# Kernel optimization log

Hardware: AMD Instinct MI355X
Metric: run time of the kernel (lower is better)

The kernel has to match this reference:

```python
import jax, jax.numpy as jnp
import numpy as np


def setup_inputs() -> dict:
    key = jax.random.key(0)
    ks = jax.random.split(key, 5)
    B, Lq, Lkv, E, H = 4, 4096, 4096, 1024, 128
    x = jax.random.normal(ks[0], (B, Lq, E), dtype=jnp.float32)
    z = jax.random.normal(ks[1], (B, Lkv, E), dtype=jnp.float32)
    s = 1.0 / np.sqrt(E)
    Wq = jax.random.normal(ks[2], (H, E), dtype=jnp.float32) * s
    Wk = jax.random.normal(ks[3], (H, E), dtype=jnp.float32) * s
    Wv = jax.random.normal(ks[4], (H, E), dtype=jnp.float32) * s
    return {"x": x, "z": z, "Wq": Wq, "Wk": Wk, "Wv": Wv}


def reference(x, z, Wq, Wk, Wv):
    # q: [B, Lq, H]; k, v: [B, Lkv, H]  (torch Linear: y = x @ W.T)
    q = jnp.einsum('bqe,he->bqh', x, Wq)
    k = jnp.einsum('bke,he->bkh', z, Wk)
    v = jnp.einsum('bke,he->bkh', z, Wv)
    # NOTE: original code MULTIPLIES by sqrt(head_dim) (faithful reproduction)
    scale = jnp.asarray(k.shape[-1], x.dtype) ** 0.5
    weights = jnp.einsum('bqh,bkh->bqk', q, k) * scale  # [B, Lq, Lkv]
    weights = jax.nn.softmax(weights, axis=-1)
    logits = jnp.einsum('bqk,bkh->bqh', weights, v)  # [B, Lq, H]
    return logits
```

## Files before the change

kernel.cpp:

```cpp
#include <hip/hip_runtime.h>

typedef __attribute__((ext_vector_type(8))) short short8;
typedef __attribute__((ext_vector_type(4))) float f32x4;
typedef __attribute__((ext_vector_type(4))) float float4v;
typedef __attribute__((ext_vector_type(4))) unsigned short ushort4v;
typedef unsigned int __attribute__((may_alias)) u32ma;

#define B_   4
#define LQ   4096
#define LKV  4096
#define E_   1024
#define H_   128
#define NSPLIT 4
#define KVSPL (LKV / NSPLIT)
#define NT    (KVSPL / 64)
#define WELEM (H_ * E_)

static __device__ __forceinline__ unsigned short bf16_rne(float f) {
    unsigned int u = __float_as_uint(f);
    u += 0x7fffu + ((u >> 16) & 1u);
    return (unsigned short)(u >> 16);
}
static __device__ __forceinline__ float bf16_tof(unsigned short h) {
    return __uint_as_float(((unsigned int)h) << 16);
}
static __device__ __forceinline__ f32x4 mfma16(short8 a, short8 b, f32x4 c) {
    return __builtin_amdgcn_mfma_f32_16x16x32_bf16(a, b, c, 0, 0, 0);
}
static __device__ __forceinline__ void gload16(const unsigned short* g, unsigned short* l) {
    __builtin_amdgcn_global_load_lds(
        (const __attribute__((address_space(1))) unsigned int*)g,
        (__attribute__((address_space(3))) unsigned int*)l, 16, 0, 0);
}

__global__ __launch_bounds__(256) void convert_w_kernel(
    const float* __restrict__ Wq, const float* __restrict__ Wk, const float* __restrict__ Wv,
    unsigned short* __restrict__ wqh, unsigned short* __restrict__ wql,
    unsigned short* __restrict__ wkh, unsigned short* __restrict__ wkl,
    unsigned short* __restrict__ wvh)
{
    const int kb = blockIdx.x;
    const int which = blockIdx.y;
    const float* W = (which == 0) ? Wq : (which == 1) ? Wk : Wv;
    unsigned short* outh = (which == 0) ? wqh : (which == 1) ? wkh : wvh;
    unsigned short* outl = (which == 0) ? wql : wkl;
    const int t = threadIdx.x;
#pragma unroll
    for (int i = 0; i < 4; ++i) {
        const int c = t * 4 + i;
        const int h = c >> 3;
        const int k = kb * 64 + (((c & 7) ^ (h & 7)) * 8);
        const float* src = W + (size_t)h * E_ + k;
        float4v v0 = *(const float4v*)(src);
        float4v v1 = *(const float4v*)(src + 4);
        short8 hi, lo;
#pragma unroll
        for (int e = 0; e < 4; ++e) {
            unsigned short h0 = bf16_rne(v0[e]);
            unsigned short h1 = bf16_rne(v1[e]);
            hi[e] = (short)h0; hi[e + 4] = (short)h1;
            lo[e] = (short)bf16_rne(v0[e] - bf16_tof(h0));
            lo[e + 4] = (short)bf16_rne(v1[e] - bf16_tof(h1));
        }
        *(short8*)&outh[(size_t)kb * 8192 + (size_t)c * 8] = hi;
        if (which < 2) *(short8*)&outl[(size_t)kb * 8192 + (size_t)c * 8] = lo;
    }
}

__global__ __launch_bounds__(512, 1) void proj_kernel(
    const float* __restrict__ x, const float* __restrict__ z,
    const unsigned short* __restrict__ wqh, const unsigned short* __restrict__ wql,
    const unsigned short* __restrict__ wkh, const unsigned short* __restrict__ wkl,
    const unsigned short* __restrict__ wvh,
    unsigned short* __restrict__ qhi, unsigned short* __restrict__ qlo,
    unsigned short* __restrict__ khi, unsigned short* __restrict__ klo,
    unsigned short* __restrict__ vt)
{
    const int bid = blockIdx.x;
    const bool qmode = bid < 128;
    const int m0 = (qmode ? bid : bid - 128) * 128;
    const float* Asrc = qmode ? x : z;
    const unsigned short* W1h = qmode ? wqh : wkh;
    const unsigned short* W1l = qmode ? wql : wkl;

    const int t = threadIdx.x;
    const int w = t >> 6, l = t & 63, lg = (l >> 4) & 3, ll = l & 15;
    const int mw = w & 3, nw = w >> 2;

    __shared__ unsigned short Ah[8192];
    __shared__ unsigned short Al[8192];
    __shared__ unsigned short Wh[2][8192];
    __shared__ unsigned short Wl[2][8192];
    __shared__ unsigned short Wv2[2][8192];

    const int ar = t >> 2, aq = t & 3;
    float4v ra[4];
    auto loadA = [&](int e0) {
        const float* p = Asrc + (size_t)(m0 + ar) * E_ + e0 + aq * 16;
#pragma unroll
        for (int i = 0; i < 4; ++i) ra[i] = *(const float4v*)(p + i * 4);
    };
    auto writeA = [&]() {
#pragma unroll
        for (int half = 0; half < 2; ++half) {
            short8 hi, lo;
#pragma unroll
            for (int e = 0; e < 4; ++e) {
                float v0 = ra[2 * half][e];
                float v1 = ra[2 * half + 1][e];
                unsigned short h0 = bf16_rne(v0);
                unsigned short h1 = bf16_rne(v1);
                hi[e] = (short)h0; hi[e + 4] = (short)h1;
                lo[e] = (short)bf16_rne(v0 - bf16_tof(h0));
                lo[e + 4] = (short)bf16_rne(v1 - bf16_tof(h1));
            }
            const int j = 2 * aq + half;
            const int off = ar * 64 + ((j ^ (ar & 7)) * 8);
            *(short8*)&Ah[off] = hi;
            *(short8*)&Al[off] = lo;
        }
    };
    auto issueW = [&](int kb, int bsel) {
#pragma unroll
        for (int i = 0; i < 2; ++i) {
            const int cbase = w * 128 + i * 64;
            const size_t so = (size_t)kb * 8192 + (size_t)(cbase + l) * 8;
            gload16(W1h + so, &Wh[bsel][(size_t)cbase * 8]);
            gload16(W1l + so, &Wl[bsel][(size_t)cbase * 8]);
            if (!qmode) gload16(wvh + so, &Wv2[bsel][(size_t)cbase * 8]);
        }
    };

    f32x4 acc[2][4], accv[2][4];
    const f32x4 zz = {0.f, 0.f, 0.f, 0.f};
#pragma unroll
    for (int rf = 0; rf < 2; ++rf)
#pragma unroll
        for (int cf = 0; cf < 4; ++cf) { acc[rf][cf] = zz; accv[rf][cf] = zz; }

    issueW(0, 0);
    loadA(0);
    writeA();
    __syncthreads();

    for (int kb = 0; kb < 16; ++kb) {
        const int bsel = kb & 1;
        if (kb < 15) { issueW(kb + 1, bsel ^ 1); loadA((kb + 1) * 64); }

#pragma unroll
        for (int ks = 0; ks < 2; ++ks) {
            short8 a_h[2], a_l[2];
#pragma unroll
            for (int rf = 0; rf < 2; ++rf) {
                const int r = mw * 32 + rf * 16 + ll;
                const int off = r * 64 + (((ks * 4 + lg) ^ (ll & 7)) * 8);
                a_h[rf] = *(const short8*)&Ah[off];
                a_l[rf] = *(const short8*)&Al[off];
            }
#pragma unroll
            for (int cf = 0; cf < 4; ++cf) {
                const int hrow = nw * 64 + cf * 16 + ll;
                const int off = hrow * 64 + (((ks * 4 + lg) ^ (ll & 7)) * 8);
                short8 bh = *(const short8*)&Wh[bsel][off];
                short8 bl = *(const short8*)&Wl[bsel][off];
#pragma unroll
                for (int rf = 0; rf < 2; ++rf) {
                    acc[rf][cf] = mfma16(a_h[rf], bh, acc[rf][cf]);
                    acc[rf][cf] = mfma16(a_h[rf], bl, acc[rf][cf]);
                    acc[rf][cf] = mfma16(a_l[rf], bh, acc[rf][cf]);
                }
                if (!qmode) {
                    short8 bv = *(const short8*)&Wv2[bsel][off];
#pragma unroll
                    for (int rf = 0; rf < 2; ++rf)
                        accv[rf][cf] = mfma16(a_h[rf], bv, accv[rf][cf]);
                }
            }
        }
        __syncthreads();
        if (kb < 15) {
            writeA();
            __syncthreads();
        }
    }

#pragma unroll
    for (int rf = 0; rf < 2; ++rf)
#pragma unroll
        for (int cf = 0; cf < 4; ++cf)
#pragma unroll
            for (int j = 0; j < 4; ++j) {
                const int m = m0 + mw * 32 + rf * 16 + 4 * lg + j;
                const int h = nw * 64 + cf * 16 + ll;
                const float val = acc[rf][cf][j];
                unsigned short hi = bf16_rne(val);
                unsigned short lo = bf16_rne(val - bf16_tof(hi));
                const size_t o = (size_t)m * H_ + h;
                if (qmode) {
                    qhi[o] = hi; qlo[o] = lo;
                } else {
                    khi[o] = hi; klo[o] = lo;
                    const int b = m >> 12, kv = m & 4095;
                    vt[(size_t)b * ((size_t)H_ * LKV) + (size_t)h * LKV + kv] =
                        bf16_rne(accv[rf][cf][j]);
                }
            }
}

__global__ __launch_bounds__(256, 2) void attn_kernel(
    const unsigned short* __restrict__ qhi, const unsigned short* __restrict__ qlo,
    const unsigned short* __restrict__ khi, const unsigned short* __restrict__ klo,
    const unsigned short* __restrict__ vt,
    float* __restrict__ Opart, float* __restrict__ msb, float* __restrict__ lsb)
{
    const int blk = blockIdx.x;
    const int bb = blk & 3;
    const int qt = (blk >> 2) & 31;
    const int split = blk >> 7;
    const int t = threadIdx.x;
    const int w = t >> 6, l = t & 63, lg = (l >> 4) & 3, ll = l & 15;

    __shared__ unsigned short Kh[8192];
    __shared__ unsigned short Kl[8192];
    __shared__ unsigned short Vb[8192];
    __shared__ unsigned short Pl[4][32][64];

    const float CSC = 11.313708498984761f * 1.4426950408889634f;

    short8 qh[2][4], ql[2][4];
#pragma unroll
    for (int b = 0; b < 2; ++b) {
        const size_t qrow = (size_t)(bb * LQ + qt * 128 + w * 32 + b * 16 + ll) * H_;
#pragma unroll
        for (int ks = 0; ks < 4; ++ks) {
            qh[b][ks] = *(const short8*)(qhi + qrow + ks * 32 + lg * 8);
            ql[b][ks] = *(const short8*)(qlo + qrow + ks * 32 + lg * 8);
        }
    }

    const int kv_base = split * KVSPL;
    const unsigned short* khb = khi + (size_t)bb * LKV * H_;
    const unsigned short* klb = klo + (size_t)bb * LKV * H_;
    const unsigned short* vbg = vt + (size_t)bb * ((size_t)H_ * LKV);

    auto issue_K = [&](int kv0) {
#pragma unroll
        for (int ci = 0; ci < 4; ++ci) {
            const int chunk = w * 4 + ci;
            const int row = chunk * 4 + (l >> 4);
            const int c = l & 15;
            const size_t so = (size_t)(kv0 + row) * H_ + ((c ^ (row & 7)) * 8);
            gload16(khb + so, &Kh[chunk * 512]);
            gload16(klb + so, &Kl[chunk * 512]);
        }
    };
    auto issue_V = [&](int kv0) {
#pragma unroll
        for (int ci = 0; ci < 4; ++ci) {
            const int chunk = w * 4 + ci;
            const int row = chunk * 8 + (l >> 3);
            const int c = l & 7;
            gload16(vbg + (size_t)row * LKV + kv0 + ((c ^ (row & 7)) * 8),
                    &Vb[chunk * 512]);
        }
    };

    f32x4 O[8][2];
    const f32x4 zz = {0.f, 0.f, 0.f, 0.f};
#pragma unroll
    for (int f = 0; f < 8; ++f) { O[f][0] = zz; O[f][1] = zz; }
    float mold[2] = {-1e30f, -1e30f};
    float lsum[2] = {0.f, 0.f};

    issue_K(kv_base);
    issue_V(kv_base);
    asm volatile("s_waitcnt vmcnt(0)" ::: "memory");
    __builtin_amdgcn_s_barrier();

    for (int ti = 0; ti < NT; ++ti) {
        f32x4 S[4][2];
#pragma unroll
        for (int a = 0; a < 4; ++a) { S[a][0] = zz; S[a][1] = zz; }
        __builtin_amdgcn_s_setprio(1);
#pragma unroll
        for (int ks = 0; ks < 4; ++ks) {
#pragma unroll
            for (int a = 0; a < 4; ++a) {
                const int row = a * 16 + ll;
                const int off = row * 128 + (((ks * 4 + lg) ^ (ll & 7)) * 8);
                short8 kh  = *(const short8*)&Kh[off];
                short8 kl2 = *(const short8*)&Kl[off];
                S[a][0] = mfma16(kh,  qh[0][ks], S[a][0]);
                S[a][0] = mfma16(kh,  ql[0][ks], S[a][0]);
                S[a][0] = mfma16(kl2, qh[0][ks], S[a][0]);
                S[a][1] = mfma16(kh,  qh[1][ks], S[a][1]);
                S[a][1] = mfma16(kh,  ql[1][ks], S[a][1]);
                S[a][1] = mfma16(kl2, qh[1][ks], S[a][1]);
            }
        }
        __builtin_amdgcn_s_setprio(0);

        float crr[2];
#pragma unroll
        for (int b = 0; b < 2; ++b) {
            float mx = S[0][b][0];
#pragma unroll
            for (int a = 0; a < 4; ++a)
#pragma unroll
                for (int j = 0; j < 4; ++j) mx = fmaxf(mx, S[a][b][j]);
            mx = fmaxf(mx, __shfl_xor(mx, 16));
            mx = fmaxf(mx, __shfl_xor(mx, 32));
            float mn = fmaxf(mold[b], mx * CSC);
            float corr = exp2f(mold[b] - mn);
            float ps = 0.f;
#pragma unroll
            for (int a = 0; a < 4; ++a) {
                float p0 = exp2f(fmaf(S[a][b][0], CSC, -mn));
                float p1 = exp2f(fmaf(S[a][b][1], CSC, -mn));
                float p2 = exp2f(fmaf(S[a][b][2], CSC, -mn));
                float p3 = exp2f(fmaf(S[a][b][3], CSC, -mn));
                ps += (p0 + p1) + (p2 + p3);
                unsigned int pk0, pk1;
                asm("v_cvt_pk_bf16_f32 %0, %1, %2" : "=v"(pk0) : "v"(p0), "v"(p1));
                asm("v_cvt_pk_bf16_f32 %0, %1, %2" : "=v"(pk1) : "v"(p2), "v"(p3));
                const int row = b * 16 + ll;
                u32ma* pd = (u32ma*)&Pl[w][0][0];
                const int di = row * 32 + (((2 * a + (lg >> 1)) ^ (ll & 7)) * 4) + 2 * (lg & 1);
                pd[di] = pk0;
                pd[di + 1] = pk1;
            }
            ps += __shfl_xor(ps, 16);
            ps += __shfl_xor(ps, 32);
            lsum[b] = lsum[b] * corr + ps;
            mold[b] = mn;
            crr[b] = corr;
        }
#pragma unroll
        for (int f = 0; f < 8; ++f) {
            O[f][0] *= crr[0];
            O[f][1] *= crr[1];
        }

        asm volatile("s_waitcnt vmcnt(0) lgkmcnt(0)" ::: "memory");
        __builtin_amdgcn_sched_barrier(0);
        __builtin_amdgcn_s_barrier();
        if (ti + 1 < NT) issue_K(kv_base + (ti + 1) * 64);
        __builtin_amdgcn_sched_barrier(0);

        __builtin_amdgcn_s_setprio(1);
#pragma unroll
        for (int ks = 0; ks < 2; ++ks) {
            short8 pb[2];
#pragma unroll
            for (int b = 0; b < 2; ++b) {
                const int row = b * 16 + ll;
                pb[b] = *(const short8*)&Pl[w][row][((ks * 4 + lg) ^ (ll & 7)) * 8];
            }
#pragma unroll
            for (int f = 0; f < 8; ++f) {
                const int row = f * 16 + ll;
                short8 va = *(const short8*)&Vb[row * 64
                                               + (((ks * 4 + lg) ^ (ll & 7)) * 8)];
                O[f][0] = mfma16(va, pb[0], O[f][0]);
                O[f][1] = mfma16(va, pb[1], O[f][1]);
            }
        }
        __builtin_amdgcn_s_setprio(0);

        __builtin_amdgcn_s_barrier();
        if (ti + 1 < NT) issue_V(kv_base + (ti + 1) * 64);
        asm volatile("s_waitcnt vmcnt(4)" ::: "memory");
        __builtin_amdgcn_sched_barrier(0);
        __builtin_amdgcn_s_barrier();
    }

    const size_t obase = ((((size_t)split * 4 + bb) * 32 + qt) * 4 + w) * 16;
#pragma unroll
    for (int f = 0; f < 8; ++f)
#pragma unroll
        for (int b = 0; b < 2; ++b)
            *(float4v*)&Opart[(obase + f * 2 + b) * 256 + l * 4] = O[f][b];

    if (lg == 0) {
#pragma unroll
        for (int b = 0; b < 2; ++b) {
            const int q = qt * 128 + w * 32 + b * 16 + ll;
            msb[((size_t)split * 4 + bb) * LQ + q] = mold[b];
            lsb[((size_t)split * 4 + bb) * LQ + q] = lsum[b];
        }
    }
}

__global__ __launch_bounds__(512) void combine_kernel(
    const float* __restrict__ Opart, const float* __restrict__ msb,
    const float* __restrict__ lsb, float* __restrict__ out)
{
    const int blk = blockIdx.x;
    const int bb = blk & 3;
    const int qt = (blk >> 2) & 31;
    const int fg = blk >> 7;
    const int t = threadIdx.x;
    const int w = t >> 6, l = t & 63, lg = (l >> 4) & 3, ll = l & 15;
    const int wq = w & 3, wf = w >> 2;

#pragma unroll
    for (int b = 0; b < 2; ++b) {
        const int q = qt * 128 + wq * 32 + b * 16 + ll;
        float ms[NSPLIT], ls[NSPLIT];
#pragma unroll
        for (int s = 0; s < NSPLIT; ++s) {
            ms[s] = msb[((size_t)s * 4 + bb) * LQ + q];
            ls[s] = lsb[((size_t)s * 4 + bb) * LQ + q];
        }
        float mM = fmaxf(fmaxf(ms[0], ms[1]), fmaxf(ms[2], ms[3]));
        float wsp[NSPLIT];
        float L = 0.f;
#pragma unroll
        for (int s = 0; s < NSPLIT; ++s) {
            wsp[s] = exp2f(ms[s] - mM);
            L += ls[s] * wsp[s];
        }
        const float inv = 1.f / L;
#pragma unroll
        for (int fi = 0; fi < 2; ++fi) {
            const int f = fg * 4 + wf * 2 + fi;
            f32x4 acc = {0.f, 0.f, 0.f, 0.f};
#pragma unroll
            for (int s = 0; s < NSPLIT; ++s) {
                const size_t ob = ((((size_t)s * 4 + bb) * 32 + qt) * 4 + wq) * 16 + f * 2 + b;
                float4v ov = *(const float4v*)&Opart[ob * 256 + l * 4];
#pragma unroll
                for (int j = 0; j < 4; ++j) acc[j] += ov[j] * wsp[s];
            }
#pragma unroll
            for (int j = 0; j < 4; ++j) acc[j] *= inv;
            *(float4v*)&out[((size_t)bb * LQ + q) * H_ + f * 16 + lg * 4] = acc;
        }
    }
}

extern "C" void kernel_launch(void* const* d_in, const int* in_sizes, int n_in,
                              void* d_out, int out_size, void* d_ws, size_t ws_size,
                              hipStream_t stream) {
    const float* x  = (const float*)d_in[0];
    const float* z  = (const float*)d_in[1];
    const float* Wq = (const float*)d_in[2];
    const float* Wk = (const float*)d_in[3];
    const float* Wv = (const float*)d_in[4];
    float* out = (float*)d_out;

    const size_t NQ = (size_t)B_ * LQ * H_;
    unsigned short* qhi = (unsigned short*)d_ws;
    unsigned short* qlo = qhi + NQ;
    unsigned short* khi = qlo + NQ;
    unsigned short* klo = khi + NQ;
    unsigned short* vtp = klo + NQ;
    float* Opart = (float*)(vtp + NQ);
    float* msb   = Opart + (size_t)NSPLIT * NQ;
    float* lsb   = msb + (size_t)NSPLIT * B_ * LQ;
    unsigned short* wqh = (unsigned short*)(lsb + (size_t)NSPLIT * B_ * LQ);
    unsigned short* wql = wqh + WELEM;
    unsigned short* wkh = wql + WELEM;
    unsigned short* wkl = wkh + WELEM;
    unsigned short* wvh = wkl + WELEM;

    convert_w_kernel<<<dim3(16, 3), 256, 0, stream>>>(Wq, Wk, Wv, wqh, wql, wkh, wkl, wvh);
    proj_kernel<<<dim3(256), 512, 0, stream>>>(x, z, wqh, wql, wkh, wkl, wvh,
                                               qhi, qlo, khi, klo, vtp);
    attn_kernel<<<dim3(512), 256, 0, stream>>>(qhi, qlo, khi, klo, vtp, Opart, msb, lsb);
    combine_kernel<<<dim3(256), 512, 0, stream>>>(Opart, msb, lsb, out);
}
```

Baseline: 138.7 us.

## Double-buffer K tiles, keep P in registers, skip unneeded softmax rescale

```diff
diff --git a/kernel.cpp b/kernel.cpp
--- a/kernel.cpp
+++ b/kernel.cpp
@@ -3,7 +3,7 @@
 typedef __attribute__((ext_vector_type(8))) short short8;
 typedef __attribute__((ext_vector_type(4))) float f32x4;
 typedef __attribute__((ext_vector_type(4))) float float4v;
-typedef __attribute__((ext_vector_type(4))) unsigned short ushort4v;
+typedef __attribute__((ext_vector_type(4))) unsigned int u32x4;
 typedef unsigned int __attribute__((may_alias)) u32ma;
 
 #define B_   4
@@ -201,7 +201,10 @@
                 } else {
                     khi[o] = hi; klo[o] = lo;
                     const int b = m >> 12, kv = m & 4095;
-                    vt[(size_t)b * ((size_t)H_ * LKV) + (size_t)h * LKV + kv] =
+                    const int kv5 = kv & 31;
+                    const int kvp = (kv & ~31) | (((kv5 >> 2) & 3) << 3)
+                                  | (((kv5 >> 4) & 1) << 2) | (kv5 & 3);
+                    vt[(size_t)b * ((size_t)H_ * LKV) + (size_t)h * LKV + kvp] =
                         bf16_rne(accv[rf][cf][j]);
                 }
             }
@@ -220,10 +223,9 @@
     const int t = threadIdx.x;
     const int w = t >> 6, l = t & 63, lg = (l >> 4) & 3, ll = l & 15;
 
-    __shared__ unsigned short Kh[8192];
-    __shared__ unsigned short Kl[8192];
+    __shared__ unsigned short Kh[2][8192];
+    __shared__ unsigned short Kl[2][8192];
     __shared__ unsigned short Vb[8192];
-    __shared__ unsigned short Pl[4][32][64];
 
     const float CSC = 11.313708498984761f * 1.4426950408889634f;
 
@@ -243,15 +245,15 @@
     const unsigned short* klb = klo + (size_t)bb * LKV * H_;
     const unsigned short* vbg = vt + (size_t)bb * ((size_t)H_ * LKV);
 
-    auto issue_K = [&](int kv0) {
+    auto issue_K = [&](int kv0, int sel) {
 #pragma unroll
         for (int ci = 0; ci < 4; ++ci) {
             const int chunk = w * 4 + ci;
             const int row = chunk * 4 + (l >> 4);
             const int c = l & 15;
             const size_t so = (size_t)(kv0 + row) * H_ + ((c ^ (row & 7)) * 8);
-            gload16(khb + so, &Kh[chunk * 512]);
-            gload16(klb + so, &Kl[chunk * 512]);
+            gload16(khb + so, &Kh[sel][chunk * 512]);
+            gload16(klb + so, &Kl[sel][chunk * 512]);
         }
     };
     auto issue_V = [&](int kv0) {
@@ -272,12 +274,16 @@
     float mold[2] = {-1e30f, -1e30f};
     float lsum[2] = {0.f, 0.f};
 
-    issue_K(kv_base);
+    issue_K(kv_base, 0);
     issue_V(kv_base);
     asm volatile("s_waitcnt vmcnt(0)" ::: "memory");
     __builtin_amdgcn_s_barrier();
 
     for (int ti = 0; ti < NT; ++ti) {
+        const int cur = ti & 1;
+        if (ti + 1 < NT) issue_K(kv_base + (ti + 1) * 64, cur ^ 1);
+        __builtin_amdgcn_sched_barrier(0);
+
         f32x4 S[4][2];
 #pragma unroll
         for (int a = 0; a < 4; ++a) { S[a][0] = zz; S[a][1] = zz; }
@@ -288,8 +294,8 @@
             for (int a = 0; a < 4; ++a) {
                 const int row = a * 16 + ll;
                 const int off = row * 128 + (((ks * 4 + lg) ^ (ll & 7)) * 8);
-                short8 kh  = *(const short8*)&Kh[off];
-                short8 kl2 = *(const short8*)&Kl[off];
+                short8 kh  = *(const short8*)&Kh[cur][off];
+                short8 kl2 = *(const short8*)&Kl[cur][off];
                 S[a][0] = mfma16(kh,  qh[0][ks], S[a][0]);
                 S[a][0] = mfma16(kh,  ql[0][ks], S[a][0]);
                 S[a][0] = mfma16(kl2, qh[0][ks], S[a][0]);
@@ -300,18 +306,19 @@
         }
         __builtin_amdgcn_s_setprio(0);
 
-        float crr[2];
+        unsigned int pw[2][8];
 #pragma unroll
         for (int b = 0; b < 2; ++b) {
-            float mx = S[0][b][0];
-#pragma unroll
-            for (int a = 0; a < 4; ++a)
-#pragma unroll
-                for (int j = 0; j < 4; ++j) mx = fmaxf(mx, S[a][b][j]);
+            float ma0 = fmaxf(fmaxf(S[0][b][0], S[0][b][1]), fmaxf(S[0][b][2], S[0][b][3]));
+            float ma1 = fmaxf(fmaxf(S[1][b][0], S[1][b][1]), fmaxf(S[1][b][2], S[1][b][3]));
+            float ma2 = fmaxf(fmaxf(S[2][b][0], S[2][b][1]), fmaxf(S[2][b][2], S[2][b][3]));
+            float ma3 = fmaxf(fmaxf(S[3][b][0], S[3][b][1]), fmaxf(S[3][b][2], S[3][b][3]));
+            float mx = fmaxf(fmaxf(ma0, ma1), fmaxf(ma2, ma3));
             mx = fmaxf(mx, __shfl_xor(mx, 16));
             mx = fmaxf(mx, __shfl_xor(mx, 32));
-            float mn = fmaxf(mold[b], mx * CSC);
-            float corr = exp2f(mold[b] - mn);
+            const float mxs = mx * CSC;
+            const bool need = !__all(mxs <= mold[b]);
+            const float mn = need ? fmaxf(mold[b], mxs) : mold[b];
             float ps = 0.f;
 #pragma unroll
             for (int a = 0; a < 4; ++a) {
@@ -323,55 +330,54 @@
                 unsigned int pk0, pk1;
                 asm("v_cvt_pk_bf16_f32 %0, %1, %2" : "=v"(pk0) : "v"(p0), "v"(p1));
                 asm("v_cvt_pk_bf16_f32 %0, %1, %2" : "=v"(pk1) : "v"(p2), "v"(p3));
-                const int row = b * 16 + ll;
-                u32ma* pd = (u32ma*)&Pl[w][0][0];
-                const int di = row * 32 + (((2 * a + (lg >> 1)) ^ (ll & 7)) * 4) + 2 * (lg & 1);
-                pd[di] = pk0;
-                pd[di + 1] = pk1;
+                pw[b][2 * a]     = pk0;
+                pw[b][2 * a + 1] = pk1;
             }
             ps += __shfl_xor(ps, 16);
             ps += __shfl_xor(ps, 32);
-            lsum[b] = lsum[b] * corr + ps;
-            mold[b] = mn;
-            crr[b] = corr;
-        }
-#pragma unroll
-        for (int f = 0; f < 8; ++f) {
-            O[f][0] *= crr[0];
-            O[f][1] *= crr[1];
-        }
-
-        asm volatile("s_waitcnt vmcnt(0) lgkmcnt(0)" ::: "memory");
+            if (need) {
+                const float corr = exp2f(mold[b] - mn);
+                lsum[b] = lsum[b] * corr + ps;
+                mold[b] = mn;
+#pragma unroll
+                for (int f = 0; f < 8; ++f) O[f][b] *= corr;
+            } else {
+                lsum[b] += ps;
+            }
+        }
+
+        asm volatile("s_waitcnt lgkmcnt(0)" ::: "memory");
+        if (ti + 1 < NT) {
+            asm volatile("s_waitcnt vmcnt(8)" ::: "memory");
+        } else {
+            asm volatile("s_waitcnt vmcnt(0)" ::: "memory");
+        }
         __builtin_amdgcn_sched_barrier(0);
         __builtin_amdgcn_s_barrier();
-        if (ti + 1 < NT) issue_K(kv_base + (ti + 1) * 64);
-        __builtin_amdgcn_sched_barrier(0);
 
         __builtin_amdgcn_s_setprio(1);
 #pragma unroll
         for (int ks = 0; ks < 2; ++ks) {
-            short8 pb[2];
-#pragma unroll
-            for (int b = 0; b < 2; ++b) {
-                const int row = b * 16 + ll;
-                pb[b] = *(const short8*)&Pl[w][row][((ks * 4 + lg) ^ (ll & 7)) * 8];
-            }
+            union { u32x4 u; short8 s; } pb0, pb1;
+            pb0.u = (u32x4){pw[0][4 * ks], pw[0][4 * ks + 1], pw[0][4 * ks + 2], pw[0][4 * ks + 3]};
+            pb1.u = (u32x4){pw[1][4 * ks], pw[1][4 * ks + 1], pw[1][4 * ks + 2], pw[1][4 * ks + 3]};
 #pragma unroll
             for (int f = 0; f < 8; ++f) {
                 const int row = f * 16 + ll;
                 short8 va = *(const short8*)&Vb[row * 64
                                                + (((ks * 4 + lg) ^ (ll & 7)) * 8)];
-                O[f][0] = mfma16(va, pb[0], O[f][0]);
-                O[f][1] = mfma16(va, pb[1], O[f][1]);
+                O[f][0] = mfma16(va, pb0.s, O[f][0]);
+                O[f][1] = mfma16(va, pb1.s, O[f][1]);
             }
         }
         __builtin_amdgcn_s_setprio(0);
 
-        __builtin_amdgcn_s_barrier();
-        if (ti + 1 < NT) issue_V(kv_base + (ti + 1) * 64);
-        asm volatile("s_waitcnt vmcnt(4)" ::: "memory");
+        asm volatile("s_waitcnt vmcnt(0) lgkmcnt(0)" ::: "memory");
         __builtin_amdgcn_sched_barrier(0);
         __builtin_amdgcn_s_barrier();
+
+        if (ti + 1 < NT) issue_V(kv_base + (ti + 1) * 64);
+        __builtin_amdgcn_sched_barrier(0);
     }
 
     const size_t obase = ((((size_t)split * 4 + bb) * 32 + qt) * 4 + w) * 16;
```

Result: no change. 140.6 us (+1.4%).
